# Kernel optimization log

Hardware: AMD Instinct MI355X
Metric: run time of the kernel (lower is better)

Reference implementation:

```python
import jax, jax.numpy as jnp
import numpy as np

WH, WW = 14, 14
NUM_HEADS = 12
NUM_REL = (2 * WH - 1) * (2 * WW - 1) + 3  # 732


def _gen_rel_pos_index(wh, ww):
    # Faithful numpy port of gen_relative_position_index (static, host-side)
    area = wh * ww
    coords = np.stack(np.meshgrid(np.arange(wh), np.arange(ww), indexing='ij'))  # (2, wh, ww)
    cf = coords.reshape(2, -1)  # (2, area)
    rel = cf[:, :, None] - cf[:, None, :]  # (2, area, area)
    rel = rel.transpose(1, 2, 0).copy()  # (area, area, 2)
    rel[..., 0] += wh - 1
    rel[..., 1] += ww - 1
    rel[..., 0] *= 2 * ww - 1
    nrd = (2 * wh - 1) * (2 * ww - 1) + 3
    idx = np.zeros((area + 1, area + 1), dtype=np.int64)
    idx[1:, 1:] = rel.sum(-1)
    idx[0, 0:] = nrd - 3
    idx[0:, 0] = nrd - 2
    idx[0, 0] = nrd - 1
    return idx


REL_IDX = jnp.asarray(_gen_rel_pos_index(WH, WW))  # (197, 197) int


def setup_inputs() -> dict:
    key = jax.random.key(0)
    k0, k1, k2, k3 = jax.random.split(key, 4)
    B, N, C = 64, WH * WW + 1, 768
    x = jax.random.normal(k0, (B, N, C), jnp.float32)
    qkv_w = jax.random.normal(k1, (3 * C, C), jnp.float32) * 0.02
    q_bias = jnp.zeros((C,), jnp.float32)
    k_bias = jnp.zeros((C,), jnp.float32)  # non-trainable buffer, always zeros
    v_bias = jnp.zeros((C,), jnp.float32)
    rel_table = jax.random.normal(k2, (NUM_REL, NUM_HEADS), jnp.float32) * 0.02
    proj_w = jax.random.normal(k3, (C, C), jnp.float32) * 0.02
    proj_b = jnp.zeros((C,), jnp.float32)
    return {"x": x, "qkv_w": qkv_w, "q_bias": q_bias, "k_bias": k_bias,
            "v_bias": v_bias, "rel_table": rel_table, "proj_w": proj_w, "proj_b": proj_b}


def reference(x, qkv_w, q_bias, k_bias, v_bias, rel_table, proj_w, proj_b):
    B, N, C = x.shape
    H = NUM_HEADS
    D = C // H
    scale = D ** -0.5
    # fused qkv projection with concatenated (q, k(zero), v) bias
    qkv_bias = jnp.concatenate([q_bias, k_bias, v_bias])
    qkv = x @ qkv_w.T + qkv_bias  # (B, N, 3C)
    qkv = qkv.reshape(B, N, 3, H, D).transpose(2, 0, 3, 1, 4)  # (3, B, H, N, D)
    q, k, v = qkv[0], qkv[1], qkv[2]
    # scores + gathered relative position bias
    attn = jnp.einsum('bhnd,bhmd->bhnm', q * scale, k)  # (B, H, N, N)
    rpb = rel_table[REL_IDX].transpose(2, 0, 1)  # (H, N, N)
    attn = jax.nn.softmax(attn + rpb[None], axis=-1)
    out = jnp.einsum('bhnm,bhmd->bhnd', attn, v)  # (B, H, N, D)
    out = out.transpose(0, 2, 1, 3).reshape(B, N, C)
    return out @ proj_w.T + proj_b
```

## Files before the change

### kernel.cpp

```cpp
#include <hip/hip_runtime.h>
#include <math.h>

#define B_   64
#define N_   197
#define C_   768
#define H_   12
#define D_   64
#define BN   12608
#define BN_PAD 12672
#define QKV_ELEMS 9682944
#define SCALE 0.125f
#define STRV 80

typedef unsigned short ushort_t;
using bf16x8  = __attribute__((ext_vector_type(8))) __bf16;
using floatx4 = __attribute__((ext_vector_type(4))) float;
using ushort8 = __attribute__((ext_vector_type(8))) unsigned short;

__device__ __forceinline__ ushort_t f2bf(float f) {
    union { float f; unsigned u; } v; v.f = f;
    unsigned r = v.u + 0x7FFF + ((v.u >> 16) & 1);
    return (ushort_t)(r >> 16);
}

__device__ __forceinline__ void gload_lds16(const void* g, void* l) {
    __builtin_amdgcn_global_load_lds(
        (const __attribute__((address_space(1))) unsigned*)g,
        (__attribute__((address_space(3))) unsigned*)l, 16, 0, 0);
}

__device__ __forceinline__ int xcd_chunk(int orig, int nwg) {
    const int q = nwg >> 3, r = nwg & 7;
    const int x = orig & 7, i = orig >> 3;
    const int base = (x < r) ? x * (q + 1) : r * (q + 1) + (x - r) * q;
    return base + i;
}

__global__ __launch_bounds__(256) void cvt_all(
    const float* __restrict__ x,  const float* __restrict__ w1,
    const float* __restrict__ w2,
    ushort_t* __restrict__ xb, ushort_t* __restrict__ wb,
    ushort_t* __restrict__ pwb)
{
    const int i = blockIdx.x * 256 + threadIdx.x;
    const float* s; ushort_t* d; int j;
    if (i < 2420736)      { s = x;  d = xb;  j = i; }
    else if (i < 2863104) { s = w1; d = wb;  j = i - 2420736; }
    else                  { s = w2; d = pwb; j = i - 2863104; }
    float4 v = ((const float4*)s)[j];
    ushort4 o;
    o.x = f2bf(v.x); o.y = f2bf(v.y); o.z = f2bf(v.z); o.w = f2bf(v.w);
    ((ushort4*)d)[j] = o;
}

__global__ __launch_bounds__(256, 4) void qkv_gemm_mfma(
    const ushort_t* __restrict__ xb,
    const ushort_t* __restrict__ wb,
    const float* __restrict__ qb,
    const float* __restrict__ kb,
    const float* __restrict__ vb,
    ushort_t* __restrict__ qkvb)
{
    __shared__ ushort_t lA[128 * 64];
    __shared__ ushort_t lB[128 * 64];
    const int t = threadIdx.x;
    const int w = t >> 6, lane = t & 63;
    const int quad = lane >> 4, li = lane & 15;
    const int wm = w >> 1, wn = w & 1;
    const int f = xcd_chunk(blockIdx.y * 18 + blockIdx.x, 18 * 99);
    const int o0 = (f % 18) * 128, m0 = (f / 18) * 128;

    floatx4 acc[4][4];
#pragma unroll
    for (int i = 0; i < 4; ++i)
#pragma unroll
        for (int j = 0; j < 4; ++j) acc[i][j] = (floatx4)0.f;

    const int rloc = lane >> 3;
    const int gdma = (lane & 7) ^ rloc;
    const int rx   = li & 7;

    for (int kt = 0; kt < 12; ++kt) {
        const int k0 = kt * 64;
#pragma unroll
        for (int s = 0; s < 4; ++s) {
            const int rb = w * 32 + s * 8;
            gload_lds16(xb + ((size_t)(m0 + rb + rloc)) * 768 + k0 + gdma * 8,
                        &lA[rb * 64]);
            gload_lds16(wb + ((size_t)(o0 + rb + rloc)) * 768 + k0 + gdma * 8,
                        &lB[rb * 64]);
        }
        __syncthreads();
#pragma unroll
        for (int kk = 0; kk < 2; ++kk) {
            bf16x8 af[4], bfr[4];
#pragma unroll
            for (int mi = 0; mi < 4; ++mi)
                af[mi] = *(const bf16x8*)
                    &lA[(wm * 64 + mi * 16 + li) * 64 + ((kk * 4 + quad) ^ rx) * 8];
#pragma unroll
            for (int ni = 0; ni < 4; ++ni)
                bfr[ni] = *(const bf16x8*)
                    &lB[(wn * 64 + ni * 16 + li) * 64 + ((kk * 4 + quad) ^ rx) * 8];
#pragma unroll
            for (int mi = 0; mi < 4; ++mi)
#pragma unroll
                for (int ni = 0; ni < 4; ++ni)
                    acc[mi][ni] = __builtin_amdgcn_mfma_f32_16x16x32_bf16(
                        af[mi], bfr[ni], acc[mi][ni], 0, 0, 0);
        }
        __syncthreads();
    }

    const int which = o0 / 768;
    const float* bias = (which == 0) ? qb : ((which == 1) ? kb : vb);
    ushort_t* dst = qkvb + (size_t)which * QKV_ELEMS;
    const float sc = (which == 0) ? SCALE : 1.0f;

#pragma unroll
    for (int mi = 0; mi < 4; ++mi) {
#pragma unroll
        for (int r = 0; r < 4; ++r) {
            const int m = m0 + wm * 64 + mi * 16 + quad * 4 + r;
            if (m < BN) {
                const int b = m / 197, n = m % 197;
#pragma unroll
                for (int ni = 0; ni < 4; ++ni) {
                    const int o  = o0 + wn * 64 + ni * 16 + li;
                    const int ol = o - which * 768;
                    const int h = ol >> 6, d = ol & 63;
                    dst[(((size_t)b * 12 + h) * 197 + n) * 64 + d] =
                        f2bf((acc[mi][ni][r] + bias[ol]) * sc);
                }
            }
        }
    }
}

__global__ __launch_bounds__(256, 4) void attn_mfma(
    const ushort_t* __restrict__ qkvb,
    const float* __restrict__ rel_table,
    ushort_t* __restrict__ aout)
{
    __shared__ ushort_t Qs[64 * 64];
    __shared__ ushort_t Ks[64 * 64];
    __shared__ ushort_t Vt[64 * STRV];
    __shared__ ushort_t Ps[64 * STRV];
    __shared__ float relh[732];

    const int f = xcd_chunk(blockIdx.y * 4 + blockIdx.x, 4 * 768);
    const int rt = f & 3, bh = f >> 2;
    const int h = bh % 12, bb = bh / 12;
    const int t = threadIdx.x;
    const int w = t >> 6, lane = t & 63, quad = lane >> 4, li = lane & 15;
    const size_t base = (size_t)bh * (197 * 64);
    const ushort_t* Qg = qkvb + base;
    const ushort_t* Kg = qkvb + (size_t)QKV_ELEMS + base;
    const ushort_t* Vg = qkvb + (size_t)2 * QKV_ELEMS + base;
    const int r0 = rt * 64;

    for (int i = t; i < 732; i += 256) relh[i] = rel_table[i * 12 + h];

    {
        const int rloc = lane >> 3, g = (lane & 7) ^ rloc;
#pragma unroll
        for (int s = 0; s < 2; ++s) {
            const int rb = (w * 2 + s) * 8;
            gload_lds16(Qg + (size_t)(r0 + rb + rloc) * 64 + g * 8, &Qs[rb * 64]);
        }
    }

    int nrow[4], p14[4], pm[4];
#pragma unroll
    for (int r = 0; r < 4; ++r) {
        const int n = r0 + w * 16 + quad * 4 + r;
        nrow[r] = n;
        const int ne = (n < 197) ? n : 0;
        const int p = (ne > 0) ? ne - 1 : 0;
        p14[r] = p / 14; pm[r] = p % 14;
    }

    float m_run[4], l_run[4];
    floatx4 accO[4];
#pragma unroll
    for (int r = 0; r < 4; ++r) { m_run[r] = -INFINITY; l_run[r] = 0.f; }
#pragma unroll
    for (int dt = 0; dt < 4; ++dt) accO[dt] = (floatx4)0.f;

    __syncthreads();

    bf16x8 aq0, aq1;
    {
        const int rq = w * 16 + li, rxq = rq & 7;
        aq0 = *(const bf16x8*)&Qs[rq * 64 + (quad ^ rxq) * 8];
        aq1 = *(const bf16x8*)&Qs[rq * 64 + ((4 + quad) ^ rxq) * 8];
    }

    for (int cc = 0; cc < 4; ++cc) {
        {
            const int rloc = lane >> 3, g = (lane & 7) ^ rloc;
#pragma unroll
            for (int s = 0; s < 2; ++s) {
                const int rb = (w * 2 + s) * 8;
                gload_lds16(Kg + (size_t)(cc * 64 + rb + rloc) * 64 + g * 8,
                            &Ks[rb * 64]);
            }
        }
        {
            const int c = lane;
            const int mg = cc * 64 + c;
            ushort8 v0, v1;
            if (mg < 197) {
                v0 = *(const ushort8*)(Vg + (size_t)mg * 64 + w * 16);
                v1 = *(const ushort8*)(Vg + (size_t)mg * 64 + w * 16 + 8);
            } else {
                v0 = (ushort8)(unsigned short)0; v1 = v0;
            }
#pragma unroll
            for (int j = 0; j < 8; ++j) Vt[(w * 16 + j) * STRV + c] = v0[j];
#pragma unroll
            for (int j = 0; j < 8; ++j) Vt[(w * 16 + 8 + j) * STRV + c] = v1[j];
        }
        __syncthreads();

        floatx4 sacc[4];
#pragma unroll
        for (int tl = 0; tl < 4; ++tl) {
            const int rk = tl * 16 + li, rxk = rk & 7;
            bf16x8 bk0 = *(const bf16x8*)&Ks[rk * 64 + (quad ^ rxk) * 8];
            bf16x8 bk1 = *(const bf16x8*)&Ks[rk * 64 + ((4 + quad) ^ rxk) * 8];
            floatx4 sa = (floatx4)0.f;
            sa = __builtin_amdgcn_mfma_f32_16x16x32_bf16(aq0, bk0, sa, 0, 0, 0);
            sa = __builtin_amdgcn_mfma_f32_16x16x32_bf16(aq1, bk1, sa, 0, 0, 0);
            sacc[tl] = sa;
        }

#pragma unroll
        for (int tl = 0; tl < 4; ++tl) {
            const int mg = cc * 64 + tl * 16 + li;
            if (mg >= 197) {
#pragma unroll
                for (int r = 0; r < 4; ++r) sacc[tl][r] = -INFINITY;
            } else {
                const int qq = (mg > 0) ? mg - 1 : 0;
                const int q14 = qq / 14, qm = qq % 14;
#pragma unroll
                for (int r = 0; r < 4; ++r) {
                    int idx;
                    const int n0 = (nrow[r] < 197) ? nrow[r] : 0;
                    if (n0 == 0 && mg == 0)      idx = 731;
                    else if (n0 == 0)            idx = 729;
                    else if (mg == 0)            idx = 730;
                    else idx = (p14[r] - q14 + 13) * 27 + (pm[r] - qm + 13);
                    sacc[tl][r] += relh[idx];
                }
            }
        }

#pragma unroll
        for (int r = 0; r < 4; ++r) {
            float mx = fmaxf(fmaxf(sacc[0][r], sacc[1][r]),
                             fmaxf(sacc[2][r], sacc[3][r]));
            mx = fmaxf(mx, __shfl_xor(mx, 1));
            mx = fmaxf(mx, __shfl_xor(mx, 2));
            mx = fmaxf(mx, __shfl_xor(mx, 4));
            mx = fmaxf(mx, __shfl_xor(mx, 8));
            const float mnew = fmaxf(m_run[r], mx);
            const float alpha = __expf(m_run[r] - mnew);
            m_run[r] = mnew;
            const float p0 = __expf(sacc[0][r] - mnew);
            const float p1 = __expf(sacc[1][r] - mnew);
            const float p2 = __expf(sacc[2][r] - mnew);
            const float p3 = __expf(sacc[3][r] - mnew);
            float rs = p0 + p1 + p2 + p3;
            rs += __shfl_xor(rs, 1);
            rs += __shfl_xor(rs, 2);
            rs += __shfl_xor(rs, 4);
            rs += __shfl_xor(rs, 8);
            l_run[r] = l_run[r] * alpha + rs;
#pragma unroll
            for (int dt = 0; dt < 4; ++dt) accO[dt][r] *= alpha;
            const int prow = w * 16 + quad * 4 + r;
            Ps[prow * STRV +  0 + li] = f2bf(p0);
            Ps[prow * STRV + 16 + li] = f2bf(p1);
            Ps[prow * STRV + 32 + li] = f2bf(p2);
            Ps[prow * STRV + 48 + li] = f2bf(p3);
        }

        {
            const int rp = w * 16 + li;
            bf16x8 pa0 = *(const bf16x8*)&Ps[rp * STRV + 0  + quad * 8];
            bf16x8 pa1 = *(const bf16x8*)&Ps[rp * STRV + 32 + quad * 8];
#pragma unroll
            for (int dt = 0; dt < 4; ++dt) {
                const int rv = dt * 16 + li;
                bf16x8 bv0 = *(const bf16x8*)&Vt[rv * STRV + 0  + quad * 8];
                bf16x8 bv1 = *(const bf16x8*)&Vt[rv * STRV + 32 + quad * 8];
                accO[dt] = __builtin_amdgcn_mfma_f32_16x16x32_bf16(
                    pa0, bv0, accO[dt], 0, 0, 0);
                accO[dt] = __builtin_amdgcn_mfma_f32_16x16x32_bf16(
                    pa1, bv1, accO[dt], 0, 0, 0);
            }
        }
        __syncthreads();
    }

#pragma unroll
    for (int r = 0; r < 4; ++r) {
        const int n = nrow[r];
        if (n < 197) {
            const float inv = 1.0f / l_run[r];
            ushort_t* op = aout + ((size_t)(bb * 197 + n)) * 768 + h * 64;
#pragma unroll
            for (int dt = 0; dt < 4; ++dt)
                op[dt * 16 + li] = f2bf(accO[dt][r] * inv);
        }
    }
}

__global__ __launch_bounds__(256, 4) void proj_gemm_mfma(
    const ushort_t* __restrict__ ab,
    const ushort_t* __restrict__ wb,
    const float* __restrict__ bias,
    float* __restrict__ out)
{
    __shared__ ushort_t lA[128 * 64];
    __shared__ ushort_t lB[128 * 64];
    const int t = threadIdx.x;
    const int w = t >> 6, lane = t & 63;
    const int quad = lane >> 4, li = lane & 15;
    const int wm = w >> 1, wn = w & 1;
    const int f = xcd_chunk(blockIdx.y * 6 + blockIdx.x, 6 * 99);
    const int o0 = (f % 6) * 128, m0 = (f / 6) * 128;

    floatx4 acc[4][4];
#pragma unroll
    for (int i = 0; i < 4; ++i)
#pragma unroll
        for (int j = 0; j < 4; ++j) acc[i][j] = (floatx4)0.f;

    const int rloc = lane >> 3;
    const int gdma = (lane & 7) ^ rloc;
    const int rx   = li & 7;

    for (int kt = 0; kt < 12; ++kt) {
        const int k0 = kt * 64;
#pragma unroll
        for (int s = 0; s < 4; ++s) {
            const int rb = w * 32 + s * 8;
            gload_lds16(ab + ((size_t)(m0 + rb + rloc)) * 768 + k0 + gdma * 8,
                        &lA[rb * 64]);
            gload_lds16(wb + ((size_t)(o0 + rb + rloc)) * 768 + k0 + gdma * 8,
                        &lB[rb * 64]);
        }
        __syncthreads();
#pragma unroll
        for (int kk = 0; kk < 2; ++kk) {
            bf16x8 af[4], bfr[4];
#pragma unroll
            for (int mi = 0; mi < 4; ++mi)
                af[mi] = *(const bf16x8*)
                    &lA[(wm * 64 + mi * 16 + li) * 64 + ((kk * 4 + quad) ^ rx) * 8];
#pragma unroll
            for (int ni = 0; ni < 4; ++ni)
                bfr[ni] = *(const bf16x8*)
                    &lB[(wn * 64 + ni * 16 + li) * 64 + ((kk * 4 + quad) ^ rx) * 8];
#pragma unroll
            for (int mi = 0; mi < 4; ++mi)
#pragma unroll
                for (int ni = 0; ni < 4; ++ni)
                    acc[mi][ni] = __builtin_amdgcn_mfma_f32_16x16x32_bf16(
                        af[mi], bfr[ni], acc[mi][ni], 0, 0, 0);
        }
        __syncthreads();
    }

#pragma unroll
    for (int mi = 0; mi < 4; ++mi) {
#pragma unroll
        for (int r = 0; r < 4; ++r) {
            const int m = m0 + wm * 64 + mi * 16 + quad * 4 + r;
            if (m < BN) {
                float* op = out + (size_t)m * 768;
#pragma unroll
                for (int ni = 0; ni < 4; ++ni) {
                    const int o = o0 + wn * 64 + ni * 16 + li;
                    op[o] = acc[mi][ni][r] + bias[o];
                }
            }
        }
    }
}

extern "C" void kernel_launch(void* const* d_in, const int* in_sizes, int n_in,
                              void* d_out, int out_size, void* d_ws, size_t ws_size,
                              hipStream_t stream)
{
    const float* x         = (const float*)d_in[0];
    const float* qkv_w     = (const float*)d_in[1];
    const float* q_bias    = (const float*)d_in[2];
    const float* k_bias    = (const float*)d_in[3];
    const float* v_bias    = (const float*)d_in[4];
    const float* rel_table = (const float*)d_in[5];
    const float* proj_w    = (const float*)d_in[6];
    const float* proj_b    = (const float*)d_in[7];
    float* out = (float*)d_out;

    char* ws = (char*)d_ws;
    ushort_t* qkvb  = (ushort_t*)ws;
    ushort_t* xb    = (ushort_t*)(ws + 58097664);
    ushort_t* aoutb = xb;
    ushort_t* wb    = (ushort_t*)(ws + 77561856);
    ushort_t* pwb   = (ushort_t*)(ws + 81100800);

    cvt_all<<<11760, 256, 0, stream>>>(x, qkv_w, proj_w, xb, wb, pwb);

    dim3 g1(18, 99);
    qkv_gemm_mfma<<<g1, 256, 0, stream>>>(xb, wb, q_bias, k_bias, v_bias, qkvb);

    dim3 g2(4, 768);
    attn_mfma<<<g2, 256, 0, stream>>>(qkvb, rel_table, aoutb);

    dim3 g3(6, 99);
    proj_gemm_mfma<<<g3, 256, 0, stream>>>(aoutb, pwb, proj_b, out);
}
```

Before: 234.9 us.

## Precompute bf16 relative-position bias tiles and stream them into attention via LDS

Adds a small kernel that expands the relative-position table into per-row-tile, per-head bf16 bias slabs in workspace, reusing the qkv weight buffer after the QKV GEMM. The attention kernel now streams the slab for each key chunk into the freed Q shared buffer with async global-to-LDS loads and adds the bias with a vector LDS read. This replaces per-element index arithmetic, divisions and scattered LDS gathers. In exchange it adds a kernel launch, extra global traffic of about 2.3 MB read per pass, an extra barrier, and bf16 rounding of the bias.

```diff
diff --git a/kernel.cpp b/kernel.cpp
--- a/kernel.cpp
+++ b/kernel.cpp
@@ -11,6 +11,7 @@
 #define QKV_ELEMS 9682944
 #define SCALE 0.125f
 #define STRV 80
+#define TPAD 72
 
 typedef unsigned short ushort_t;
 using bf16x8  = __attribute__((ext_vector_type(8))) __bf16;
@@ -21,6 +22,11 @@
     union { float f; unsigned u; } v; v.f = f;
     unsigned r = v.u + 0x7FFF + ((v.u >> 16) & 1);
     return (ushort_t)(r >> 16);
+}
+
+__device__ __forceinline__ float bf2f(ushort_t u) {
+    union { unsigned u; float f; } v; v.u = ((unsigned)u) << 16;
+    return v.f;
 }
 
 __device__ __forceinline__ void gload_lds16(const void* g, void* l) {
@@ -53,6 +59,33 @@
     ((ushort4*)d)[j] = o;
 }
 
+__global__ __launch_bounds__(256) void build_rpb(
+    const float* __restrict__ rel_table,
+    ushort_t* __restrict__ t4)
+{
+    const int p = blockIdx.x * 256 + threadIdx.x;
+    if (p >= 4 * 197 * TPAD) return;
+    const int nl = p % TPAD;
+    const int rest = p / TPAD;
+    const int m = rest % 197, rt = rest / 197;
+    const int n = rt * 64 + nl;
+    const bool valid = (n < 197);
+    int idx = 0;
+    if (valid) {
+        if (n == 0 && m == 0)      idx = 731;
+        else if (n == 0)           idx = 729;
+        else if (m == 0)           idx = 730;
+        else {
+            const int pp = n - 1, qq = m - 1;
+            idx = (pp / 14 - qq / 14 + 13) * 27 + (pp % 14 - qq % 14 + 13);
+        }
+    }
+#pragma unroll
+    for (int h = 0; h < 12; ++h)
+        t4[((size_t)(rt * 12 + h) * 197 + m) * TPAD + nl] =
+            valid ? f2bf(rel_table[idx * 12 + h]) : (ushort_t)0;
+}
+
 __global__ __launch_bounds__(256, 4) void qkv_gemm_mfma(
     const ushort_t* __restrict__ xb,
     const ushort_t* __restrict__ wb,
@@ -139,14 +172,13 @@
 
 __global__ __launch_bounds__(256, 4) void attn_mfma(
     const ushort_t* __restrict__ qkvb,
-    const float* __restrict__ rel_table,
+    const ushort_t* __restrict__ t4,
     ushort_t* __restrict__ aout)
 {
-    __shared__ ushort_t Qs[64 * 64];
+    __shared__ ushort_t Qs[64 * TPAD];
     __shared__ ushort_t Ks[64 * 64];
     __shared__ ushort_t Vt[64 * STRV];
     __shared__ ushort_t Ps[64 * STRV];
-    __shared__ float relh[732];
 
     const int f = xcd_chunk(blockIdx.y * 4 + blockIdx.x, 4 * 768);
     const int rt = f & 3, bh = f >> 2;
@@ -158,8 +190,7 @@
     const ushort_t* Kg = qkvb + (size_t)QKV_ELEMS + base;
     const ushort_t* Vg = qkvb + (size_t)2 * QKV_ELEMS + base;
     const int r0 = rt * 64;
-
-    for (int i = t; i < 732; i += 256) relh[i] = rel_table[i * 12 + h];
+    const ushort_t* slab = t4 + (size_t)(rt * 12 + h) * (197 * TPAD);
 
     {
         const int rloc = lane >> 3, g = (lane & 7) ^ rloc;
@@ -170,15 +201,9 @@
         }
     }
 
-    int nrow[4], p14[4], pm[4];
-#pragma unroll
-    for (int r = 0; r < 4; ++r) {
-        const int n = r0 + w * 16 + quad * 4 + r;
-        nrow[r] = n;
-        const int ne = (n < 197) ? n : 0;
-        const int p = (ne > 0) ? ne - 1 : 0;
-        p14[r] = p / 14; pm[r] = p % 14;
-    }
+    int nrow[4];
+#pragma unroll
+    for (int r = 0; r < 4; ++r) nrow[r] = r0 + w * 16 + quad * 4 + r;
 
     float m_run[4], l_run[4];
     floatx4 accO[4];
@@ -195,6 +220,7 @@
         aq0 = *(const bf16x8*)&Qs[rq * 64 + (quad ^ rxq) * 8];
         aq1 = *(const bf16x8*)&Qs[rq * 64 + ((4 + quad) ^ rxq) * 8];
     }
+    __syncthreads();
 
     for (int cc = 0; cc < 4; ++cc) {
         {
@@ -206,6 +232,9 @@
                             &Ks[rb * 64]);
             }
         }
+        for (int c = w; c < 9; c += 4)
+            gload_lds16(slab + (size_t)cc * 4608 + c * 512 + lane * 8,
+                        &Qs[c * 512]);
         {
             const int c = lane;
             const int mg = cc * 64 + c;
@@ -242,18 +271,12 @@
 #pragma unroll
                 for (int r = 0; r < 4; ++r) sacc[tl][r] = -INFINITY;
             } else {
-                const int qq = (mg > 0) ? mg - 1 : 0;
-                const int q14 = qq / 14, qm = qq % 14;
-#pragma unroll
-                for (int r = 0; r < 4; ++r) {
-                    int idx;
-                    const int n0 = (nrow[r] < 197) ? nrow[r] : 0;
-                    if (n0 == 0 && mg == 0)      idx = 731;
-                    else if (n0 == 0)            idx = 729;
-                    else if (mg == 0)            idx = 730;
-                    else idx = (p14[r] - q14 + 13) * 27 + (pm[r] - qm + 13);
-                    sacc[tl][r] += relh[idx];
-                }
+                ushort4 bv = *(const ushort4*)
+                    &Qs[(tl * 16 + li) * TPAD + w * 16 + quad * 4];
+                sacc[tl][0] += bf2f(bv.x);
+                sacc[tl][1] += bf2f(bv.y);
+                sacc[tl][2] += bf2f(bv.z);
+                sacc[tl][3] += bf2f(bv.w);
             }
         }
 
@@ -411,6 +434,7 @@
     ushort_t* xb    = (ushort_t*)(ws + 58097664);
     ushort_t* aoutb = xb;
     ushort_t* wb    = (ushort_t*)(ws + 77561856);
+    ushort_t* t4b   = wb;
     ushort_t* pwb   = (ushort_t*)(ws + 81100800);
 
     cvt_all<<<11760, 256, 0, stream>>>(x, qkv_w, proj_w, xb, wb, pwb);
@@ -418,8 +442,10 @@
     dim3 g1(18, 99);
     qkv_gemm_mfma<<<g1, 256, 0, stream>>>(xb, wb, q_bias, k_bias, v_bias, qkvb);
 
+    build_rpb<<<222, 256, 0, stream>>>(rel_table, t4b);
+
     dim3 g2(4, 768);
-    attn_mfma<<<g2, 256, 0, stream>>>(qkvb, rel_table, aoutb);
+    attn_mfma<<<g2, 256, 0, stream>>>(qkvb, t4b, aoutb);
 
     dim3 g3(6, 99);
     proj_gemm_mfma<<<g3, 256, 0, stream>>>(aoutb, pwb, proj_b, out);
```

After: 235.4 us. About the same (+0.2%).
